# Kernel optimization log

Hardware: AMD Instinct MI355X
Metric: run time of the kernel (lower is better)

## Reference

```python
import jax, jax.numpy as jnp
import numpy as np
import math

B, SQ, SK, EMB = 4, 2048, 2048, 1024
HEAD, QK, V = 16, 64, 64


def setup_inputs() -> dict:
    key = jax.random.key(0)
    ks = jax.random.split(key, 9)
    s = 1.0 / math.sqrt(EMB)
    return {
        "x_q": jax.random.normal(ks[0], (B, SQ, EMB), dtype=jnp.float32),
        "x_k_v": jax.random.normal(ks[1], (B, SK, EMB), dtype=jnp.float32),
        "attn_mask": jax.random.randint(ks[2], (B, SQ, SK), 0, 2) == 1,
        "w_q": jax.random.uniform(ks[3], (EMB, HEAD * QK), jnp.float32, -s, s),
        "b_q": jax.random.uniform(ks[4], (HEAD * QK,), jnp.float32, -s, s),
        "w_k": jax.random.uniform(ks[5], (EMB, HEAD * QK), jnp.float32, -s, s),
        "b_k": jax.random.uniform(ks[6], (HEAD * QK,), jnp.float32, -s, s),
        "w_v": jax.random.uniform(ks[7], (EMB, HEAD * V), jnp.float32, -s, s),
        "b_v": jax.random.uniform(ks[8], (HEAD * V,), jnp.float32, -s, s),
    }


def reference(x_q, x_k_v, attn_mask, w_q, b_q, w_k, b_k, w_v, b_v):
    # projections: [B,S,H*D] -> [B,H,S,D]
    q = (x_q @ w_q + b_q).reshape(B, SQ, HEAD, QK).transpose(0, 2, 1, 3)
    k = (x_k_v @ w_k + b_k).reshape(B, SK, HEAD, QK).transpose(0, 2, 1, 3)
    v = (x_k_v @ w_v + b_v).reshape(B, SK, HEAD, V).transpose(0, 2, 1, 3)
    # scores: [B,H,SQ,SK]
    attn = jnp.einsum("bhqd,bhkd->bhqk", q, k) / math.sqrt(QK)
    attn = jnp.where(attn_mask[:, None, :, :], -1e9, attn)
    attn = jax.nn.softmax(attn, axis=-1)
    z = jnp.einsum("bhqk,bhkd->bhqd", attn, v)  # [B,H,SQ,V]
    return z.transpose(0, 2, 1, 3).reshape(B, SQ, HEAD * V)
```

## Files before the change

### kernel.cpp

```cpp
#include <hip/hip_runtime.h>
#include <hip/hip_bf16.h>
#include <stdint.h>

#define BB 4
#define SQL 2048
#define SKL 2048
#define EMB 1024
#define NH 16
#define DH 64

typedef __bf16 bf16x8 __attribute__((ext_vector_type(8)));
typedef short s16x4 __attribute__((ext_vector_type(4)));
typedef float f32x4 __attribute__((ext_vector_type(4)));

#define QSCALE 0.1803368801111144f

__device__ __forceinline__ unsigned short f2bf(float f) {
  union { float f; uint32_t u; } v; v.f = f;
  uint32_t u = v.u;
  return (unsigned short)((u + 0x7fffu + ((u >> 16) & 1u)) >> 16);
}

typedef const __attribute__((address_space(1))) void* gas_t;
typedef __attribute__((address_space(3))) void* las_t;
__device__ __forceinline__ void gld16(const void* g, void* l) {
  __builtin_amdgcn_global_load_lds((gas_t)g, (las_t)l, 16, 0, 0);
}

__global__ void cvt_bf16_kernel(const float* __restrict__ src,
                                unsigned short* __restrict__ dst, int n4) {
  int i = blockIdx.x * 256 + threadIdx.x;
  if (i >= n4) return;
  float4 v = ((const float4*)src)[i];
  ushort4 o;
  o.x = f2bf(v.x); o.y = f2bf(v.y); o.z = f2bf(v.z); o.w = f2bf(v.w);
  ((ushort4*)dst)[i] = o;
}

__global__ void wtrans_kernel(const float* __restrict__ w0, const float* __restrict__ w1,
                              const float* __restrict__ w2,
                              unsigned short* __restrict__ o0, unsigned short* __restrict__ o1,
                              unsigned short* __restrict__ o2) {
  __shared__ float t[32][33];
  const float* w = blockIdx.z == 0 ? w0 : (blockIdx.z == 1 ? w1 : w2);
  unsigned short* o = blockIdx.z == 0 ? o0 : (blockIdx.z == 1 ? o1 : o2);
  int tx = threadIdx.x & 31, ty = threadIdx.x >> 5;
  int n0 = blockIdx.x * 32, k0 = blockIdx.y * 32;
#pragma unroll
  for (int r = 0; r < 4; r++)
    t[ty + r * 8][tx] = w[(size_t)(k0 + ty + r * 8) * EMB + n0 + tx];
  __syncthreads();
#pragma unroll
  for (int r = 0; r < 4; r++)
    o[(size_t)(n0 + ty + r * 8) * EMB + k0 + tx] = f2bf(t[tx][ty + r * 8]);
}

__global__ void maskpack_kernel(const int* __restrict__ m, unsigned int* __restrict__ words) {
  int w = blockIdx.x * 256 + threadIdx.x;
  const int4* p = (const int4*)(m + (size_t)w * 32);
  unsigned int bits = 0;
#pragma unroll
  for (int j = 0; j < 8; j++) {
    int4 v = p[j];
    bits |= (v.x != 0 ? 1u : 0u) << (j * 4 + 0);
    bits |= (v.y != 0 ? 1u : 0u) << (j * 4 + 1);
    bits |= (v.z != 0 ? 1u : 0u) << (j * 4 + 2);
    bits |= (v.w != 0 ? 1u : 0u) << (j * 4 + 3);
  }
  words[w] = bits;
}

__global__ __launch_bounds__(256, 2) void proj_gemm_kernel(
    const unsigned short* __restrict__ Aq, const unsigned short* __restrict__ Akv,
    const unsigned short* __restrict__ W0, const unsigned short* __restrict__ W1,
    const unsigned short* __restrict__ W2,
    const float* __restrict__ bq, const float* __restrict__ bk, const float* __restrict__ bv,
    unsigned short* __restrict__ Oq, unsigned short* __restrict__ Ok,
    unsigned short* __restrict__ Ov) {
  __shared__ short As[128 * 32];
  __shared__ short Bs[128 * 32];
  const int z = blockIdx.z;
  const unsigned short* A = (z == 0) ? Aq : Akv;
  const unsigned short* Bt = (z == 0) ? W0 : (z == 1 ? W1 : W2);
  const float* bias = (z == 0) ? bq : (z == 1 ? bk : bv);
  unsigned short* out = (z == 0) ? Oq : (z == 1 ? Ok : Ov);
  const float oscale = (z == 0) ? QSCALE : 1.0f;

  const int tid = threadIdx.x;
  const int wave = tid >> 6, lane = tid & 63;
  const int l15 = lane & 15, q4 = lane >> 4;
  const int wm = wave >> 1, wn = wave & 1;
  const int m0 = blockIdx.y * 128, n0 = blockIdx.x * 128;

  f32x4 acc[4][4];
#pragma unroll
  for (int i = 0; i < 4; i++)
#pragma unroll
    for (int j = 0; j < 4; j++) acc[i][j] = (f32x4){0.f, 0.f, 0.f, 0.f};

  const int r = tid >> 2;
  const int c = (tid & 3) * 8;
  const unsigned short* gA0 = A + (size_t)(m0 + r) * EMB + c;
  const unsigned short* gA1 = A + (size_t)(m0 + r + 64) * EMB + c;
  const unsigned short* gB0 = Bt + (size_t)(n0 + r) * EMB + c;
  const unsigned short* gB1 = Bt + (size_t)(n0 + r + 64) * EMB + c;
  short* lA0 = As + tid * 8;
  short* lA1 = As + tid * 8 + 2048;
  short* lB0 = Bs + tid * 8;
  short* lB1 = Bs + tid * 8 + 2048;

  for (int kt = 0; kt < EMB / 32; kt++) {
    __syncthreads();
    gld16(gA0 + kt * 32, lA0);
    gld16(gA1 + kt * 32, lA1);
    gld16(gB0 + kt * 32, lB0);
    gld16(gB1 + kt * 32, lB1);
    __syncthreads();
    bf16x8 a[4], b[4];
#pragma unroll
    for (int i = 0; i < 4; i++)
      a[i] = *(const bf16x8*)(As + (wm * 64 + i * 16 + l15) * 32 + q4 * 8);
#pragma unroll
    for (int j = 0; j < 4; j++)
      b[j] = *(const bf16x8*)(Bs + (wn * 64 + j * 16 + l15) * 32 + q4 * 8);
#pragma unroll
    for (int i = 0; i < 4; i++)
#pragma unroll
      for (int j = 0; j < 4; j++)
        acc[i][j] = __builtin_amdgcn_mfma_f32_16x16x32_bf16(a[i], b[j], acc[i][j], 0, 0, 0);
  }

#pragma unroll
  for (int i = 0; i < 4; i++) {
    const int mrow = m0 + wm * 64 + i * 16 + q4 * 4;
#pragma unroll
    for (int j = 0; j < 4; j++) {
      const int n = n0 + wn * 64 + j * 16 + l15;
      const float bvv = bias[n];
      const int h = n >> 6, d = n & 63;
      if (z <= 1) {
#pragma unroll
        for (int rg = 0; rg < 4; rg++) {
          int m = mrow + rg;
          int bb = m >> 11, sq = m & 2047;
          out[(size_t)((bb * NH + h) * SQL + sq) * DH + d] = f2bf((acc[i][j][rg] + bvv) * oscale);
        }
      } else {
        int bb = mrow >> 11, sq = mrow & 2047;
        ushort4 pk;
        pk.x = f2bf(acc[i][j][0] + bvv);
        pk.y = f2bf(acc[i][j][1] + bvv);
        pk.z = f2bf(acc[i][j][2] + bvv);
        pk.w = f2bf(acc[i][j][3] + bvv);
        *(ushort4*)(out + (size_t)((bb * NH + h) * DH + d) * SKL + sq) = pk;
      }
    }
  }
}

__global__ __launch_bounds__(256, 4) void attn_kernel(
    const unsigned short* __restrict__ Qb,
    const unsigned short* __restrict__ Kb,
    const unsigned short* __restrict__ Vt,
    const unsigned int* __restrict__ mw,
    float* __restrict__ out) {
  __shared__ short Ks[64 * 64];
  __shared__ short Vs[64 * 64];
  __shared__ float Ls[4][16];
  const int tid = threadIdx.x;
  const int wave = tid >> 6, lane = tid & 63;
  const int l15 = lane & 15, q4 = lane >> 4;
  const int bh = blockIdx.y, b = bh >> 4, h = bh & 15;
  const int q0 = blockIdx.x * 64 + wave * 16;

  const unsigned short* qg = Qb + (size_t)(bh * SQL + q0 + l15) * DH + q4 * 8;
  const bf16x8 qa0 = *(const bf16x8*)qg;
  const bf16x8 qa1 = *(const bf16x8*)(qg + 32);

  f32x4 o[4];
#pragma unroll
  for (int j = 0; j < 4; j++) o[j] = (f32x4){0.f, 0.f, 0.f, 0.f};
  float lrow = 0.f;

  const int sr = tid >> 3;
  const int gc8 = ((tid & 7) ^ (sr & 7)) * 8;
  const unsigned short* kgA = Kb + (size_t)bh * SKL * DH + sr * DH + gc8;
  const unsigned short* kgB = Kb + (size_t)bh * SKL * DH + (sr + 32) * DH + gc8;
  const unsigned short* vgA = Vt + (size_t)bh * DH * SKL + (size_t)sr * SKL + gc8;
  const unsigned short* vgB = Vt + (size_t)bh * DH * SKL + (size_t)(sr + 32) * SKL + gc8;
  short* lK0 = Ks + tid * 8; short* lK1 = Ks + 2048 + tid * 8;
  short* lV0 = Vs + tid * 8; short* lV1 = Vs + 2048 + tid * 8;

  const int lx = l15 & 7;
  const int kph0 = (q4 ^ lx) * 8;
  const int kph1 = ((q4 + 4) ^ lx) * 8;
  const int voff = (q4 & 1) * 4;
  const unsigned int* mrp = mw + ((size_t)b * SQL + q0 + l15) * 64;

  for (int kv0 = 0; kv0 < SKL; kv0 += 64) {
    __syncthreads();
    gld16(kgA + kv0 * DH, lK0);
    gld16(kgB + kv0 * DH, lK1);
    gld16(vgA + kv0, lV0);
    gld16(vgB + kv0, lV1);
    uint2 mk = *(const uint2*)(mrp + (kv0 >> 5));
    __syncthreads();

#pragma unroll
    for (int sub = 0; sub < 4; sub++) {
      const short* kbase = Ks + (sub * 16 + l15) * 64;
      bf16x8 af0 = *(const bf16x8*)(kbase + kph0);
      bf16x8 af1 = *(const bf16x8*)(kbase + kph1);
      f32x4 s4 = (f32x4){0.f, 0.f, 0.f, 0.f};
      s4 = __builtin_amdgcn_mfma_f32_16x16x32_bf16(af0, qa0, s4, 0, 0, 0);
      s4 = __builtin_amdgcn_mfma_f32_16x16x32_bf16(af1, qa1, s4, 0, 0, 0);

      unsigned int mbits = ((sub & 2) ? mk.y : mk.x) >> (((sub & 1) * 16) + q4 * 4);
      float p[4];
#pragma unroll
      for (int rg = 0; rg < 4; rg++) {
        float e = __builtin_exp2f(s4[rg]);
        e = ((mbits >> rg) & 1u) ? 0.f : e;
        lrow += e;
        p[rg] = e;
      }
      union { float f; uint32_t u; } c0, c1, c2, c3;
      c0.f = p[0]; c1.f = p[1]; c2.f = p[2]; c3.f = p[3];
      uint32_t lo = ((c0.u + 0x8000u) >> 16) | ((c1.u + 0x8000u) & 0xffff0000u);
      uint32_t hi = ((c2.u + 0x8000u) >> 16) | ((c3.u + 0x8000u) & 0xffff0000u);
      uint2 ppu; ppu.x = lo; ppu.y = hi;
      s16x4 pp = __builtin_bit_cast(s16x4, ppu);

      const int vph = ((sub * 2 + (q4 >> 1)) ^ lx) * 8 + voff;
#pragma unroll
      for (int dsub = 0; dsub < 4; dsub++) {
        s16x4 bv = *(const s16x4*)(Vs + (dsub * 16 + l15) * 64 + vph);
        o[dsub] = __builtin_amdgcn_mfma_f32_16x16x16bf16_1k(pp, bv, o[dsub], 0, 0, 0);
      }
    }
  }

  lrow += __shfl_xor(lrow, 16);
  lrow += __shfl_xor(lrow, 32);
  if (lane < 16) Ls[wave][lane] = lrow;
  __syncthreads();

#pragma unroll
  for (int rg = 0; rg < 4; rg++) {
    const float inv = 1.0f / Ls[wave][q4 * 4 + rg];
    float* op = out + (size_t)(b * SQL + q0 + q4 * 4 + rg) * 1024 + h * DH + l15;
#pragma unroll
    for (int dsub = 0; dsub < 4; dsub++) op[dsub * 16] = o[dsub][rg] * inv;
  }
}

extern "C" void kernel_launch(void* const* d_in, const int* in_sizes, int n_in,
                              void* d_out, int out_size, void* d_ws, size_t ws_size,
                              hipStream_t stream) {
  const float* x_q  = (const float*)d_in[0];
  const float* x_kv = (const float*)d_in[1];
  const int*   amask = (const int*)d_in[2];
  const float* w_q  = (const float*)d_in[3];
  const float* b_q  = (const float*)d_in[4];
  const float* w_k  = (const float*)d_in[5];
  const float* b_k  = (const float*)d_in[6];
  const float* w_v  = (const float*)d_in[7];
  const float* b_v  = (const float*)d_in[8];
  float* out = (float*)d_out;

  char* ws = (char*)d_ws;
  unsigned short* xq_bf  = (unsigned short*)(ws + 0);
  unsigned short* xkv_bf = (unsigned short*)(ws + 16777216);
  unsigned short* wqt    = (unsigned short*)(ws + 33554432);
  unsigned short* wkt    = (unsigned short*)(ws + 35651584);
  unsigned short* wvt    = (unsigned short*)(ws + 37748736);
  unsigned short* Qb     = (unsigned short*)(ws + 39845888);
  unsigned short* Kb     = (unsigned short*)(ws + 56623104);
  unsigned short* Vtb    = (unsigned short*)(ws + 73400320);
  unsigned int*   mwords = (unsigned int*)(ws + 90177536);

  cvt_bf16_kernel<<<8192, 256, 0, stream>>>(x_q, xq_bf, 2097152);
  cvt_bf16_kernel<<<8192, 256, 0, stream>>>(x_kv, xkv_bf, 2097152);
  wtrans_kernel<<<dim3(32, 32, 3), 256, 0, stream>>>(w_q, w_k, w_v, wqt, wkt, wvt);
  maskpack_kernel<<<2048, 256, 0, stream>>>(amask, mwords);
  proj_gemm_kernel<<<dim3(8, 64, 3), 256, 0, stream>>>(
      xq_bf, xkv_bf, wqt, wkt, wvt, b_q, b_k, b_v, Qb, Kb, Vtb);
  attn_kernel<<<dim3(32, 64), 256, 0, stream>>>(Qb, Kb, Vtb, mwords, out);
}
```

Baseline: 396.1 us.

## Pre-swizzle V into MFMA fragment layout, stream K from global, expand mask

The V projection epilogue now writes V directly in the per-lane MFMA fragment order, in 64-key chunks. Attention can then load each chunk linearly into double-buffered LDS, overlapping the next load with compute. K fragments are read straight from global memory instead of being staged through LDS. The mask is expanded to 16-bit AND-masks applied to the packed bf16 probabilities, and the row sum comes from an extra MFMA against a ones vector instead of a scalar accumulation plus shuffle reduction. The cost is a mask buffer 16 times larger, with much more mask traffic, and K reads that go through cache separately for each wave.

```diff
diff --git a/kernel.cpp b/kernel.cpp
--- a/kernel.cpp
+++ b/kernel.cpp
@@ -55,19 +55,18 @@
     o[(size_t)(n0 + ty + r * 8) * EMB + k0 + tx] = f2bf(t[tx][ty + r * 8]);
 }
 
-__global__ void maskpack_kernel(const int* __restrict__ m, unsigned int* __restrict__ words) {
-  int w = blockIdx.x * 256 + threadIdx.x;
-  const int4* p = (const int4*)(m + (size_t)w * 32);
-  unsigned int bits = 0;
+__global__ void maskf_kernel(const int* __restrict__ m, unsigned int* __restrict__ w) {
+  int t = blockIdx.x * 256 + threadIdx.x;
+  const int4* p = (const int4*)(m + (size_t)t * 32);
+  unsigned int* dst = w + (size_t)t * 16;
 #pragma unroll
   for (int j = 0; j < 8; j++) {
     int4 v = p[j];
-    bits |= (v.x != 0 ? 1u : 0u) << (j * 4 + 0);
-    bits |= (v.y != 0 ? 1u : 0u) << (j * 4 + 1);
-    bits |= (v.z != 0 ? 1u : 0u) << (j * 4 + 2);
-    bits |= (v.w != 0 ? 1u : 0u) << (j * 4 + 3);
-  }
-  words[w] = bits;
+    unsigned int w0 = (v.x ? 0u : 0xffffu) | (v.y ? 0u : 0xffff0000u);
+    unsigned int w1 = (v.z ? 0u : 0xffffu) | (v.w ? 0u : 0xffff0000u);
+    dst[j * 2] = w0;
+    dst[j * 2 + 1] = w1;
+  }
 }
 
 __global__ __launch_bounds__(256, 2) void proj_gemm_kernel(
@@ -147,12 +146,16 @@
         }
       } else {
         int bb = mrow >> 11, sq = mrow & 2047;
+        int chunk = sq >> 6, r64 = sq & 63;
+        int sub = r64 >> 4, q4v = (r64 >> 2) & 3;
+        int dsub = d >> 4, l15v = d & 15;
+        int slot = ((sub * 4 + dsub) << 6) + q4v * 16 + l15v;
         ushort4 pk;
         pk.x = f2bf(acc[i][j][0] + bvv);
         pk.y = f2bf(acc[i][j][1] + bvv);
         pk.z = f2bf(acc[i][j][2] + bvv);
         pk.w = f2bf(acc[i][j][3] + bvv);
-        *(ushort4*)(out + (size_t)((bb * NH + h) * DH + d) * SKL + sq) = pk;
+        *(ushort4*)(out + (size_t)(bb * NH + h) * (SKL * DH) + chunk * 4096 + slot * 4) = pk;
       }
     }
   }
@@ -161,12 +164,10 @@
 __global__ __launch_bounds__(256, 4) void attn_kernel(
     const unsigned short* __restrict__ Qb,
     const unsigned short* __restrict__ Kb,
-    const unsigned short* __restrict__ Vt,
+    const unsigned short* __restrict__ Vg,
     const unsigned int* __restrict__ mw,
     float* __restrict__ out) {
-  __shared__ short Ks[64 * 64];
-  __shared__ short Vs[64 * 64];
-  __shared__ float Ls[4][16];
+  __shared__ short Vs[2 * 4096];
   const int tid = threadIdx.x;
   const int wave = tid >> 6, lane = tid & 63;
   const int l15 = lane & 15, q4 = lane >> 4;
@@ -180,74 +181,63 @@
   f32x4 o[4];
 #pragma unroll
   for (int j = 0; j < 4; j++) o[j] = (f32x4){0.f, 0.f, 0.f, 0.f};
-  float lrow = 0.f;
-
-  const int sr = tid >> 3;
-  const int gc8 = ((tid & 7) ^ (sr & 7)) * 8;
-  const unsigned short* kgA = Kb + (size_t)bh * SKL * DH + sr * DH + gc8;
-  const unsigned short* kgB = Kb + (size_t)bh * SKL * DH + (sr + 32) * DH + gc8;
-  const unsigned short* vgA = Vt + (size_t)bh * DH * SKL + (size_t)sr * SKL + gc8;
-  const unsigned short* vgB = Vt + (size_t)bh * DH * SKL + (size_t)(sr + 32) * SKL + gc8;
-  short* lK0 = Ks + tid * 8; short* lK1 = Ks + 2048 + tid * 8;
-  short* lV0 = Vs + tid * 8; short* lV1 = Vs + 2048 + tid * 8;
-
-  const int lx = l15 & 7;
-  const int kph0 = (q4 ^ lx) * 8;
-  const int kph1 = ((q4 + 4) ^ lx) * 8;
-  const int voff = (q4 & 1) * 4;
-  const unsigned int* mrp = mw + ((size_t)b * SQL + q0 + l15) * 64;
-
-  for (int kv0 = 0; kv0 < SKL; kv0 += 64) {
-    __syncthreads();
-    gld16(kgA + kv0 * DH, lK0);
-    gld16(kgB + kv0 * DH, lK1);
-    gld16(vgA + kv0, lV0);
-    gld16(vgB + kv0, lV1);
-    uint2 mk = *(const uint2*)(mrp + (kv0 >> 5));
-    __syncthreads();
+  f32x4 osum = (f32x4){0.f, 0.f, 0.f, 0.f};
+  const s16x4 ones = (s16x4){0x3f80, 0x3f80, 0x3f80, 0x3f80};
+
+  const unsigned short* vgb = Vg + (size_t)bh * (SKL * DH);
+  const unsigned short* kcb = Kb + (size_t)bh * (SKL * DH) + (size_t)(l15)*64 + q4 * 8;
+  const unsigned int* mrp = mw + ((size_t)b * SQL + q0 + l15) * 1024 + q4 * 2;
+
+  gld16(vgb + tid * 8, Vs + tid * 8);
+  gld16(vgb + 2048 + tid * 8, Vs + 2048 + tid * 8);
+  __syncthreads();
+
+  for (int cch = 0; cch < 32; cch++) {
+    const int buf = cch & 1;
+    if (cch < 31) {
+      const unsigned short* src = vgb + (size_t)(cch + 1) * 4096 + tid * 8;
+      short* dst = Vs + (buf ^ 1) * 4096 + tid * 8;
+      gld16(src, dst);
+      gld16(src + 2048, dst + 2048);
+    }
+
+    const unsigned short* kc = kcb + (size_t)cch * 4096;
+    const short* vlane = Vs + buf * 4096 + lane * 4;
+    const unsigned int* mc = mrp + cch * 32;
 
 #pragma unroll
     for (int sub = 0; sub < 4; sub++) {
-      const short* kbase = Ks + (sub * 16 + l15) * 64;
-      bf16x8 af0 = *(const bf16x8*)(kbase + kph0);
-      bf16x8 af1 = *(const bf16x8*)(kbase + kph1);
+      const unsigned short* kr = kc + sub * 1024;
+      bf16x8 af0 = *(const bf16x8*)kr;
+      bf16x8 af1 = *(const bf16x8*)(kr + 32);
       f32x4 s4 = (f32x4){0.f, 0.f, 0.f, 0.f};
       s4 = __builtin_amdgcn_mfma_f32_16x16x32_bf16(af0, qa0, s4, 0, 0, 0);
       s4 = __builtin_amdgcn_mfma_f32_16x16x32_bf16(af1, qa1, s4, 0, 0, 0);
 
-      unsigned int mbits = ((sub & 2) ? mk.y : mk.x) >> (((sub & 1) * 16) + q4 * 4);
-      float p[4];
-#pragma unroll
-      for (int rg = 0; rg < 4; rg++) {
-        float e = __builtin_exp2f(s4[rg]);
-        e = ((mbits >> rg) & 1u) ? 0.f : e;
-        lrow += e;
-        p[rg] = e;
-      }
-      union { float f; uint32_t u; } c0, c1, c2, c3;
-      c0.f = p[0]; c1.f = p[1]; c2.f = p[2]; c3.f = p[3];
-      uint32_t lo = ((c0.u + 0x8000u) >> 16) | ((c1.u + 0x8000u) & 0xffff0000u);
-      uint32_t hi = ((c2.u + 0x8000u) >> 16) | ((c3.u + 0x8000u) & 0xffff0000u);
+      uint2 mk = *(const uint2*)(mc + sub * 8);
+      union { float f; uint32_t u; } e0, e1, e2, e3;
+      e0.f = __builtin_exp2f(s4[0]);
+      e1.f = __builtin_exp2f(s4[1]);
+      e2.f = __builtin_exp2f(s4[2]);
+      e3.f = __builtin_exp2f(s4[3]);
+      uint32_t lo = (((e0.u + 0x8000u) >> 16) | ((e1.u + 0x8000u) & 0xffff0000u)) & mk.x;
+      uint32_t hi = (((e2.u + 0x8000u) >> 16) | ((e3.u + 0x8000u) & 0xffff0000u)) & mk.y;
       uint2 ppu; ppu.x = lo; ppu.y = hi;
       s16x4 pp = __builtin_bit_cast(s16x4, ppu);
 
-      const int vph = ((sub * 2 + (q4 >> 1)) ^ lx) * 8 + voff;
-#pragma unroll
-      for (int dsub = 0; dsub < 4; dsub++) {
-        s16x4 bv = *(const s16x4*)(Vs + (dsub * 16 + l15) * 64 + vph);
-        o[dsub] = __builtin_amdgcn_mfma_f32_16x16x16bf16_1k(pp, bv, o[dsub], 0, 0, 0);
-      }
+      const short* vf = vlane + sub * 1024;
+      o[0] = __builtin_amdgcn_mfma_f32_16x16x16bf16_1k(pp, *(const s16x4*)(vf + 0), o[0], 0, 0, 0);
+      o[1] = __builtin_amdgcn_mfma_f32_16x16x16bf16_1k(pp, *(const s16x4*)(vf + 256), o[1], 0, 0, 0);
+      o[2] = __builtin_amdgcn_mfma_f32_16x16x16bf16_1k(pp, *(const s16x4*)(vf + 512), o[2], 0, 0, 0);
+      o[3] = __builtin_amdgcn_mfma_f32_16x16x16bf16_1k(pp, *(const s16x4*)(vf + 768), o[3], 0, 0, 0);
+      osum = __builtin_amdgcn_mfma_f32_16x16x16bf16_1k(pp, ones, osum, 0, 0, 0);
     }
-  }
-
-  lrow += __shfl_xor(lrow, 16);
-  lrow += __shfl_xor(lrow, 32);
-  if (lane < 16) Ls[wave][lane] = lrow;
-  __syncthreads();
+    __syncthreads();
+  }
 
 #pragma unroll
   for (int rg = 0; rg < 4; rg++) {
-    const float inv = 1.0f / Ls[wave][q4 * 4 + rg];
+    const float inv = 1.0f / osum[rg];
     float* op = out + (size_t)(b * SQL + q0 + q4 * 4 + rg) * 1024 + h * DH + l15;
 #pragma unroll
     for (int dsub = 0; dsub < 4; dsub++) op[dsub * 16] = o[dsub][rg] * inv;
@@ -276,14 +266,14 @@
   unsigned short* wvt    = (unsigned short*)(ws + 37748736);
   unsigned short* Qb     = (unsigned short*)(ws + 39845888);
   unsigned short* Kb     = (unsigned short*)(ws + 56623104);
-  unsigned short* Vtb    = (unsigned short*)(ws + 73400320);
-  unsigned int*   mwords = (unsigned int*)(ws + 90177536);
+  unsigned short* Vgb    = (unsigned short*)(ws + 73400320);
+  unsigned int*   M32    = (unsigned int*)(ws + 0);
 
   cvt_bf16_kernel<<<8192, 256, 0, stream>>>(x_q, xq_bf, 2097152);
   cvt_bf16_kernel<<<8192, 256, 0, stream>>>(x_kv, xkv_bf, 2097152);
   wtrans_kernel<<<dim3(32, 32, 3), 256, 0, stream>>>(w_q, w_k, w_v, wqt, wkt, wvt);
-  maskpack_kernel<<<2048, 256, 0, stream>>>(amask, mwords);
   proj_gemm_kernel<<<dim3(8, 64, 3), 256, 0, stream>>>(
-      xq_bf, xkv_bf, wqt, wkt, wvt, b_q, b_k, b_v, Qb, Kb, Vtb);
-  attn_kernel<<<dim3(32, 64), 256, 0, stream>>>(Qb, Kb, Vtb, mwords, out);
-}
+      xq_bf, xkv_bf, wqt, wkt, wvt, b_q, b_k, b_v, Qb, Kb, Vgb);
+  maskf_kernel<<<2048, 256, 0, stream>>>(amask, M32);
+  attn_kernel<<<dim3(32, 64), 256, 0, stream>>>(Qb, Kb, Vgb, M32, out);
+}
```

New measurement: 667.7 us. 1.69x slower.
